# Kernel optimization log

Measured on AMD Instinct MI355X. Metric: run time of the kernel, lower is better.

The kernel has to match this reference:

```python
import jax, jax.numpy as jnp
import numpy as np

NUM_NODES = 50000
NUM_EDGES = 800000
NUM_LABEL_EDGES = 100000
F_IN, F_HID, F_OUT = 128, 128, 64


def gcn_conv(x, src, dst, W, b, n):
    # PyG GCNConv: h = x @ W; add self-loops; symmetric normalization
    # deg counted on destination (col), including self-loop (+1).
    h = x @ W
    deg = jax.ops.segment_sum(jnp.ones(src.shape, h.dtype), dst, num_segments=n) + 1.0
    dinv = jax.lax.rsqrt(deg)  # deg >= 1 always (self-loop)
    norm = dinv[src] * dinv[dst]                       # [E]
    agg = jax.ops.segment_sum(h[src] * norm[:, None], dst, num_segments=n)
    agg = agg + h * (dinv * dinv)[:, None]             # self-loop term dinv[i]^2 * h[i]
    return agg + b


def setup_inputs() -> dict:
    key = jax.random.key(0)
    ks = jax.random.split(key, 9)
    x = jax.random.normal(ks[0], (NUM_NODES, F_IN), dtype=jnp.float32)
    edge_index = jax.random.randint(ks[1], (2, NUM_EDGES), 0, NUM_NODES, dtype=jnp.int64)
    edge_label_index = jax.random.randint(ks[2], (2, NUM_LABEL_EDGES), 0, NUM_NODES, dtype=jnp.int64)
    def glorot(k, fi, fo):
        s = (6.0 / (fi + fo)) ** 0.5
        return jax.random.uniform(k, (fi, fo), jnp.float32, -s, s)
    return {
        "x": x,
        "edge_index": edge_index,
        "edge_label_index": edge_label_index,
        "W1": glorot(ks[3], F_IN, F_HID),  "b1": jnp.zeros((F_HID,), jnp.float32),
        "W2": glorot(ks[4], F_HID, F_HID), "b2": jnp.zeros((F_HID,), jnp.float32),
        "W3": glorot(ks[5], F_HID, F_OUT), "b3": jnp.zeros((F_OUT,), jnp.float32),
    }


def reference(x, edge_index, edge_label_index, W1, b1, W2, b2, W3, b3):
    src, dst = edge_index[0], edge_index[1]
    z = jax.nn.relu(gcn_conv(x, src, dst, W1, b1, NUM_NODES))
    z = jax.nn.relu(gcn_conv(z, src, dst, W2, b2, NUM_NODES))
    z = gcn_conv(z, src, dst, W3, b3, NUM_NODES)
    # decode: dot product of endpoint embeddings per label edge
    return jnp.sum(z[edge_label_index[0]] * z[edge_label_index[1]], axis=-1)
```

## Files before the change

kernel.cpp:

```cpp
#include <hip/hip_runtime.h>
#include <hip/hip_bf16.h>
#include <stdint.h>

#define NN 50000
#define NE 800000
#define NL 100000
#define SLOTS 64

#define NB 196
#define BSH 8
#define BCAP 5376

typedef __attribute__((ext_vector_type(8))) short bf16x8;
typedef __attribute__((ext_vector_type(4))) float f32x4;
typedef __attribute__((ext_vector_type(4))) unsigned int u32x4;
typedef __attribute__((ext_vector_type(2))) unsigned int u32x2;
typedef __attribute__((ext_vector_type(8))) unsigned short u16x8;

__device__ __forceinline__ float asf(unsigned int u) {
    union { unsigned int i; float f; } c; c.i = u; return c.f;
}
__device__ __forceinline__ float bflo(unsigned int x) { return asf(x << 16); }
__device__ __forceinline__ float bfhi(unsigned int x) { return asf(x & 0xffff0000u); }
__device__ __forceinline__ unsigned short f2bf(float f) {
    union { float f; unsigned int i; } c; c.f = f;
    unsigned int u = c.i + (0x7fffu + ((c.i >> 16) & 1u));
    return (unsigned short)(u >> 16);
}

__global__ void k_wprep(const float* __restrict__ W1, const float* __restrict__ W2,
                        const float* __restrict__ W3, unsigned short* __restrict__ Wt,
                        int* __restrict__ cursor) {
    int idx = blockIdx.x * 256 + threadIdx.x;
    if (idx < NB) cursor[idx] = 0;
    const float* W; unsigned short* O; int base, Mloc;
    if (idx < 16384)      { W = W1; O = Wt;         base = idx;         Mloc = 128; }
    else if (idx < 32768) { W = W2; O = Wt + 16384; base = idx - 16384; Mloc = 128; }
    else                  { W = W3; O = Wt + 32768; base = idx - 32768; Mloc = 64;  }
    int n = base >> 7, k = base & 127;
    O[base] = f2bf(W[k * Mloc + n]);
}

__global__ __launch_bounds__(256) void k_bin(
        const int* __restrict__ src, const int* __restrict__ dst,
        int* __restrict__ cursor, unsigned int* __restrict__ binbuf) {
    __shared__ int hcnt[NB];
    __shared__ int hbase[NB];
    __shared__ unsigned int epk[2048];
    int tid = threadIdx.x;
    if (tid < NB) hcnt[tid] = 0;
    __syncthreads();
    int e0 = blockIdx.x * 2048;
    int e1 = min(e0 + 2048, NE);
    for (int e = e0 + tid; e < e1; e += 256) {
        int d = dst[e], s = src[e];
        atomicAdd(&hcnt[d >> BSH], 1);
        epk[e - e0] = (unsigned int)s | ((unsigned int)d << 16);
    }
    __syncthreads();
    if (tid < NB) { hbase[tid] = atomicAdd(&cursor[tid], hcnt[tid]); hcnt[tid] = 0; }
    __syncthreads();
    for (int e = e0 + tid; e < e1; e += 256) {
        unsigned int pk = epk[e - e0];
        int b = (int)(pk >> 16) >> BSH;
        int p = hbase[b] + atomicAdd(&hcnt[b], 1);
        if (p < BCAP)
            __builtin_nontemporal_store(pk, &binbuf[(size_t)b * BCAP + p]);
    }
}

__global__ __launch_bounds__(256) void k_csr(
        const unsigned int* __restrict__ binbuf, const int* __restrict__ cursor,
        int* __restrict__ deg, unsigned short* __restrict__ colp) {
    __shared__ unsigned short lcol[256 * SLOTS];
    __shared__ int ldeg[256];
    int tid = threadIdx.x;
    int blk = blockIdx.x;
    int base = blk << BSH;
    int nNodes = min(256, NN - base);
    ldeg[tid] = 0;
    u32x4* lz = (u32x4*)lcol;
#pragma unroll
    for (int i = 0; i < 8; ++i) lz[i * 256 + tid] = (u32x4){0, 0, 0, 0};
    __syncthreads();
    int cnt = min(cursor[blk], BCAP);
    for (int e = tid; e < cnt; e += 256) {
        unsigned int pk = __builtin_nontemporal_load(&binbuf[(size_t)blk * BCAP + e]);
        int d = (int)(pk >> 16) - base;
        int p = atomicAdd(&ldeg[d], 1);
        if (p < SLOTS) {
            int pp = (p < 32) ? ((p & 3) * 8 + (p >> 2)) : p;
            lcol[d * SLOTS + pp] = (unsigned short)(pk & 0xffffu);
        }
    }
    __syncthreads();
    if (tid < nNodes) deg[base + tid] = ldeg[tid];
    u32x4* gout = (u32x4*)(colp + (size_t)base * SLOTS);
    const u32x4* lin = (const u32x4*)lcol;
    for (int i = tid; i < nNodes * 8; i += 256) gout[i] = lin[i];
}

__global__ __launch_bounds__(256) void k_gemm1(
        const float* __restrict__ A, const unsigned short* __restrict__ Wt,
        const int* __restrict__ deg, unsigned short* __restrict__ Outb, int N) {
    constexpr int K = 128;
    constexpr int NT = 8;
    int tid = threadIdx.x;
    int lane = tid & 63, wave = tid >> 6;
    int m = lane & 15, quad = lane >> 4;
    int rowA = blockIdx.x * 64 + wave * 16 + m;
    int rA = min(rowA, N - 1);

    bf16x8 afr[4];
    const float* p = A + (size_t)rA * K + quad * 8;
#pragma unroll
    for (int s = 0; s < 4; ++s) {
        float4 lo = *(const float4*)(p + s * 32);
        float4 hi = *(const float4*)(p + s * 32 + 4);
        bf16x8 r;
        r[0] = (short)f2bf(lo.x); r[1] = (short)f2bf(lo.y);
        r[2] = (short)f2bf(lo.z); r[3] = (short)f2bf(lo.w);
        r[4] = (short)f2bf(hi.x); r[5] = (short)f2bf(hi.y);
        r[6] = (short)f2bf(hi.z); r[7] = (short)f2bf(hi.w);
        afr[s] = r;
    }

    f32x4 acc[NT];
#pragma unroll
    for (int t = 0; t < NT; ++t) { acc[t][0] = 0.f; acc[t][1] = 0.f; acc[t][2] = 0.f; acc[t][3] = 0.f; }
#pragma unroll
    for (int t = 0; t < NT; ++t) {
        const unsigned short* wp = Wt + (size_t)(t * 16 + m) * K + quad * 8;
#pragma unroll
        for (int s = 0; s < 4; ++s) {
            bf16x8 bfr = *(const bf16x8*)(wp + s * 32);
            acc[t] = __builtin_amdgcn_mfma_f32_16x16x32_bf16(afr[s], bfr, acc[t], 0, 0, 0);
        }
    }

    int outRowBase = blockIdx.x * 64 + wave * 16 + quad * 4;
    float di[4];
#pragma unroll
    for (int i = 0; i < 4; ++i) di[i] = rsqrtf((float)deg[min(outRowBase + i, N - 1)] + 1.0f);
#pragma unroll
    for (int t = 0; t < NT; ++t)
#pragma unroll
        for (int i = 0; i < 4; ++i) {
            int rr = outRowBase + i;
            if (rr < N) Outb[(size_t)rr * 128 + t * 16 + m] = f2bf(acc[t][i] * di[i]);
        }
}

template <int M_>
__global__ __launch_bounds__(256, 8) void k_agg_gemm(
        const unsigned short* __restrict__ hs, const int* __restrict__ deg,
        const unsigned short* __restrict__ colp, const float* __restrict__ bias,
        const unsigned short* __restrict__ Wt, unsigned short* __restrict__ Outb) {
    constexpr int K = 128;
    constexpr int NT = M_ / 64;
    __shared__ __align__(16) unsigned short As[16][136];
    int tid = threadIdx.x;
    int lane = tid & 63, wave = tid >> 6;
    int tileBase = blockIdx.x * 16;
    int g = lane >> 4, c = lane & 15;
    const unsigned short* hc = hs + c * 8;
    int nodeB = tileBase + wave * 4;

    int degv[4], cnt[4];
#pragma unroll
    for (int t = 0; t < 4; ++t) { degv[t] = deg[nodeB + t]; cnt[t] = min(degv[t], SLOTS); }

    u16x8 sl = *(const u16x8*)(colp + (unsigned)nodeB * SLOTS + g * 8);
    unsigned int smk = (g == 0) ? 0xffffffffu : 0u;

#pragma unroll
    for (int t = 0; t < 4; ++t) {
        int r = wave * 4 + t;
        int node = nodeB + t;

        u32x4 sv = *(const u32x4*)(hc + (unsigned)node * K);
        u32x4 vv[4];
#pragma unroll
        for (int k2 = 0; k2 < 4; ++k2)
            vv[k2] = *(const u32x4*)(hc + (unsigned)sl[k2] * K);
        u16x8 sln = sl;
        if (t < 3) sln = *(const u16x8*)(colp + (unsigned)(node + 1) * SLOTS + g * 8);

        float acc[8];
#pragma unroll
        for (int k = 0; k < 4; ++k) {
            unsigned int xv = sv[k] & smk;
            acc[2 * k] = bflo(xv); acc[2 * k + 1] = bfhi(xv);
        }
#pragma unroll
        for (int k2 = 0; k2 < 4; ++k2) {
            unsigned int mk = (4 * k2 + g < cnt[t]) ? 0xffffffffu : 0u;
#pragma unroll
            for (int k = 0; k < 4; ++k) {
                unsigned int xv = vv[k2][k] & mk;
                acc[2 * k] += bflo(xv); acc[2 * k + 1] += bfhi(xv);
            }
        }
        if (cnt[t] > 16) {
#pragma unroll
            for (int k2 = 0; k2 < 4; ++k2)
                vv[k2] = *(const u32x4*)(hc + (unsigned)sl[k2 + 4] * K);
#pragma unroll
            for (int k2 = 0; k2 < 4; ++k2) {
                unsigned int mk = (16 + 4 * k2 + g < cnt[t]) ? 0xffffffffu : 0u;
#pragma unroll
                for (int k = 0; k < 4; ++k) {
                    unsigned int xv = vv[k2][k] & mk;
                    acc[2 * k] += bflo(xv); acc[2 * k + 1] += bfhi(xv);
                }
            }
        }
        if (cnt[t] > 32) {
            int mi = (lane < cnt[t]) ? (int)colp[(unsigned)node * SLOTS + lane] : 0;
            for (int j = 32; j < cnt[t]; j += 4) {
                int i0 = __shfl(mi, j + g, 64);
                u32x4 v0 = {0, 0, 0, 0};
                if (j + g < cnt[t]) v0 = *(const u32x4*)(hc + (unsigned)i0 * K);
#pragma unroll
                for (int k = 0; k < 4; ++k) {
                    acc[2 * k] += bflo(v0[k]); acc[2 * k + 1] += bfhi(v0[k]);
                }
            }
        }
        sl = sln;

#pragma unroll
        for (int k = 0; k < 8; ++k) {
            acc[k] += __shfl_xor(acc[k], 16, 64);
            acc[k] += __shfl_xor(acc[k], 32, 64);
        }
        if (g == 0) {
            float di = rsqrtf((float)degv[t] + 1.0f);
            const float4* bp = (const float4*)(bias + c * 8);
            float4 b0 = bp[0], b1 = bp[1];
            float bb[8] = {b0.x, b0.y, b0.z, b0.w, b1.x, b1.y, b1.z, b1.w};
            u32x4 pv;
#pragma unroll
            for (int k = 0; k < 4; ++k) {
                float o0 = fmaxf(di * acc[2 * k]     + bb[2 * k],     0.f);
                float o1 = fmaxf(di * acc[2 * k + 1] + bb[2 * k + 1], 0.f);
                pv[k] = (unsigned int)f2bf(o0) | ((unsigned int)f2bf(o1) << 16);
            }
            *(u32x4*)&As[r][c * 8] = pv;
        }
    }
    __syncthreads();

    int m = lane & 15, quad = lane >> 4;
    bf16x8 afr[4];
#pragma unroll
    for (int s = 0; s < 4; ++s)
        afr[s] = *(const bf16x8*)&As[m][s * 32 + quad * 8];

    f32x4 gacc[NT];
#pragma unroll
    for (int t = 0; t < NT; ++t) { gacc[t][0] = 0.f; gacc[t][1] = 0.f; gacc[t][2] = 0.f; gacc[t][3] = 0.f; }
#pragma unroll
    for (int t = 0; t < NT; ++t) {
        int ct = wave * NT + t;
        const unsigned short* wp = Wt + (size_t)(ct * 16 + m) * K + quad * 8;
#pragma unroll
        for (int s = 0; s < 4; ++s) {
            bf16x8 bfr = *(const bf16x8*)(wp + s * 32);
            gacc[t] = __builtin_amdgcn_mfma_f32_16x16x32_bf16(afr[s], bfr, gacc[t], 0, 0, 0);
        }
    }

    int rowBase = tileBase + quad * 4;
    float di[4];
#pragma unroll
    for (int i = 0; i < 4; ++i) di[i] = rsqrtf((float)deg[rowBase + i] + 1.0f);
#pragma unroll
    for (int t = 0; t < NT; ++t) {
        int ct = wave * NT + t;
#pragma unroll
        for (int i = 0; i < 4; ++i)
            Outb[(size_t)(rowBase + i) * M_ + ct * 16 + m] = f2bf(gacc[t][i] * di[i]);
    }
}

__global__ __launch_bounds__(256, 8) void k_agg64(
        const unsigned short* __restrict__ hs, const int* __restrict__ deg,
        const unsigned short* __restrict__ colp, const float* __restrict__ bias,
        unsigned short* __restrict__ out, int n) {
    int tid = threadIdx.x;
    int wave = tid >> 6, lane = tid & 63;
    int node = blockIdx.x * 4 + wave;
    int g = lane >> 4, c = lane & 15;
    const unsigned short* hc = hs + c * 4;

    int degv = deg[node];
    int cnt = min(degv, SLOTS);
    u16x8 sl = *(const u16x8*)(colp + (unsigned)node * SLOTS + g * 8);

    u32x2 sv = *(const u32x2*)(hc + (unsigned)node * 64);
    u32x2 vv[4];
#pragma unroll
    for (int k2 = 0; k2 < 4; ++k2)
        vv[k2] = *(const u32x2*)(hc + (unsigned)sl[k2] * 64);

    unsigned int smk = (g == 0) ? 0xffffffffu : 0u;
    float acc[4];
#pragma unroll
    for (int k = 0; k < 2; ++k) {
        unsigned int xv = sv[k] & smk;
        acc[2 * k] = bflo(xv); acc[2 * k + 1] = bfhi(xv);
    }
#pragma unroll
    for (int k2 = 0; k2 < 4; ++k2) {
        unsigned int mk = (4 * k2 + g < cnt) ? 0xffffffffu : 0u;
#pragma unroll
        for (int k = 0; k < 2; ++k) {
            unsigned int xv = vv[k2][k] & mk;
            acc[2 * k] += bflo(xv); acc[2 * k + 1] += bfhi(xv);
        }
    }
    if (cnt > 16) {
#pragma unroll
        for (int k2 = 0; k2 < 4; ++k2)
            vv[k2] = *(const u32x2*)(hc + (unsigned)sl[k2 + 4] * 64);
#pragma unroll
        for (int k2 = 0; k2 < 4; ++k2) {
            unsigned int mk = (16 + 4 * k2 + g < cnt) ? 0xffffffffu : 0u;
#pragma unroll
            for (int k = 0; k < 2; ++k) {
                unsigned int xv = vv[k2][k] & mk;
                acc[2 * k] += bflo(xv); acc[2 * k + 1] += bfhi(xv);
            }
        }
    }
    if (cnt > 32) {
        int mi = (lane < cnt) ? (int)colp[(unsigned)node * SLOTS + lane] : 0;
        for (int j = 32; j < cnt; j += 4) {
            int i0 = __shfl(mi, j + g, 64);
            u32x2 v0 = {0, 0};
            if (j + g < cnt) v0 = *(const u32x2*)(hc + (unsigned)i0 * 64);
#pragma unroll
            for (int k = 0; k < 2; ++k) {
                acc[2 * k] += bflo(v0[k]); acc[2 * k + 1] += bfhi(v0[k]);
            }
        }
    }
#pragma unroll
    for (int k = 0; k < 4; ++k) {
        acc[k] += __shfl_xor(acc[k], 16, 64);
        acc[k] += __shfl_xor(acc[k], 32, 64);
    }
    if (g == 0) {
        float di = rsqrtf((float)degv + 1.0f);
        float4 bb = *(const float4*)(bias + c * 4);
        u32x2 pv;
        pv[0] = (unsigned int)f2bf(di * acc[0] + bb.x) |
                ((unsigned int)f2bf(di * acc[1] + bb.y) << 16);
        pv[1] = (unsigned int)f2bf(di * acc[2] + bb.z) |
                ((unsigned int)f2bf(di * acc[3] + bb.w) << 16);
        *(u32x2*)(out + (size_t)node * 64 + c * 4) = pv;
    }
}

__global__ __launch_bounds__(256) void k_decode(
        const unsigned short* __restrict__ z, const int* __restrict__ ls,
        const int* __restrict__ ld, float* __restrict__ out, int nl) {
    int tid = threadIdx.x;
    int lane = tid & 63, wave = tid >> 6;
    int g = lane >> 3, c = lane & 7;
    int e = (blockIdx.x * 4 + wave) * 4 + (g >> 1);
    int row = (g & 1) ? ld[e] : ls[e];
    u32x4 v = *(const u32x4*)(z + (size_t)row * 64 + c * 8);
    u32x4 w;
#pragma unroll
    for (int k = 0; k < 4; ++k) w[k] = (unsigned int)__shfl_xor((int)v[k], 8, 64);
    float p = 0.f;
#pragma unroll
    for (int k = 0; k < 4; ++k)
        p += bflo(v[k]) * bflo(w[k]) + bfhi(v[k]) * bfhi(w[k]);
    p += __shfl_xor(p, 1, 64);
    p += __shfl_xor(p, 2, 64);
    p += __shfl_xor(p, 4, 64);
    if ((lane & 15) == 0) out[e] = p;
}


static inline size_t align256(size_t x) { return (x + 255) & ~(size_t)255; }

extern "C" void kernel_launch(void* const* d_in, const int* in_sizes, int n_in,
                              void* d_out, int out_size, void* d_ws, size_t ws_size,
                              hipStream_t stream) {
    const float* x  = (const float*)d_in[0];
    const int*   ei = (const int*)d_in[1];
    const int*   li = (const int*)d_in[2];
    const float* W1 = (const float*)d_in[3];
    const float* b1 = (const float*)d_in[4];
    const float* W2 = (const float*)d_in[5];
    const float* b2 = (const float*)d_in[6];
    const float* W3 = (const float*)d_in[7];
    const float* b3 = (const float*)d_in[8];
    float* out = (float*)d_out;

    const int* src = ei;
    const int* dst = ei + NE;
    const int* ls = li;
    const int* ld = li + NL;

    char* ws = (char*)d_ws;
    size_t off = 0;
    int* deg    = (int*)(ws + off); off += align256(NN * 4);
    int* cursor = (int*)(ws + off); off += align256(NB * 4);
    unsigned int* binbuf = (unsigned int*)(ws + off); off += align256((size_t)NB * BCAP * 4);
    unsigned short* colp = (unsigned short*)(ws + off); off += align256((size_t)NN * SLOTS * 2);
    unsigned short* Wtb  = (unsigned short*)(ws + off); off += align256(40960 * 2);
    unsigned short* bufA = (unsigned short*)(ws + off); off += align256((size_t)NN * 128 * 2);
    unsigned short* bufB = (unsigned short*)(ws + off); off += align256((size_t)NN * 128 * 2);
    unsigned short* bufZ = (unsigned short*)(ws + off); off += align256((size_t)NN * 64 * 2);

    k_wprep<<<160, 256, 0, stream>>>(W1, W2, W3, Wtb, cursor);
    k_bin<<<391, 256, 0, stream>>>(src, dst, cursor, binbuf);
    k_csr<<<NB, 256, 0, stream>>>(binbuf, cursor, deg, colp);

    k_gemm1<<<782, 256, 0, stream>>>(x, Wtb, deg, bufA, NN);
    k_agg_gemm<128><<<3125, 256, 0, stream>>>(bufA, deg, colp, b1, Wtb + 16384, bufB);
    k_agg_gemm<64><<<3125, 256, 0, stream>>>(bufB, deg, colp, b2, Wtb + 32768, bufA);
    k_agg64<<<12500, 256, 0, stream>>>(bufA, deg, colp, b3, bufZ, NN);
    k_decode<<<6250, 256, 0, stream>>>(bufZ, ls, ld, out, NL);
}
```

Measured before the change: 251.2 us.

## Fold self-loops into padded neighbor slots and gather branchlessly

The CSR build now fills empty neighbor slots with a sentinel index that points at a zeroed pad row, and writes each node's own index into the slot right after its last neighbor. The aggregation kernels can then gather a fixed first block of 24 slots with no masking and no separate self-term load, and the tail paths for high-degree nodes are unrolled. The layer-3 input buffer is offset inside bufA so that the 64-wide pad row lands on the already-zeroed row. The cost is always loading 24 slots, even for low-degree nodes, in exchange for removing per-element masks and branches.

```diff
diff --git a/kernel.cpp b/kernel.cpp
--- a/kernel.cpp
+++ b/kernel.cpp
@@ -6,6 +6,7 @@
 #define NE 800000
 #define NL 100000
 #define SLOTS 64
+#define PADROW 50000
 
 #define NB 196
 #define BSH 8
@@ -30,9 +31,12 @@
 
 __global__ void k_wprep(const float* __restrict__ W1, const float* __restrict__ W2,
                         const float* __restrict__ W3, unsigned short* __restrict__ Wt,
-                        int* __restrict__ cursor) {
+                        int* __restrict__ cursor, unsigned int* __restrict__ padA,
+                        unsigned int* __restrict__ padB) {
     int idx = blockIdx.x * 256 + threadIdx.x;
     if (idx < NB) cursor[idx] = 0;
+    if (idx < 64) padA[idx] = 0;
+    else if (idx < 128) padB[idx - 64] = 0;
     const float* W; unsigned short* O; int base, Mloc;
     if (idx < 16384)      { W = W1; O = Wt;         base = idx;         Mloc = 128; }
     else if (idx < 32768) { W = W2; O = Wt + 16384; base = idx - 16384; Mloc = 128; }
@@ -79,9 +83,11 @@
     int base = blk << BSH;
     int nNodes = min(256, NN - base);
     ldeg[tid] = 0;
+    const unsigned int fw = 0xC350C350u;
+    u32x4 fill = {fw, fw, fw, fw};
     u32x4* lz = (u32x4*)lcol;
 #pragma unroll
-    for (int i = 0; i < 8; ++i) lz[i * 256 + tid] = (u32x4){0, 0, 0, 0};
+    for (int i = 0; i < 8; ++i) lz[i * 256 + tid] = fill;
     __syncthreads();
     int cnt = min(cursor[blk], BCAP);
     for (int e = tid; e < cnt; e += 256) {
@@ -94,7 +100,15 @@
         }
     }
     __syncthreads();
-    if (tid < nNodes) deg[base + tid] = ldeg[tid];
+    if (tid < nNodes) {
+        int dv = ldeg[tid];
+        deg[base + tid] = dv;
+        if (dv < SLOTS) {
+            int pp = (dv < 32) ? ((dv & 3) * 8 + (dv >> 2)) : dv;
+            lcol[tid * SLOTS + pp] = (unsigned short)(base + tid);
+        }
+    }
+    __syncthreads();
     u32x4* gout = (u32x4*)(colp + (size_t)base * SLOTS);
     const u32x4* lin = (const u32x4*)lcol;
     for (int i = tid; i < nNodes * 8; i += 256) gout[i] = lin[i];
@@ -166,64 +180,54 @@
     const unsigned short* hc = hs + c * 8;
     int nodeB = tileBase + wave * 4;
 
-    int degv[4], cnt[4];
-#pragma unroll
-    for (int t = 0; t < 4; ++t) { degv[t] = deg[nodeB + t]; cnt[t] = min(degv[t], SLOTS); }
+    int4 dg = *(const int4*)(deg + nodeB);
+    int dgv[4] = {dg.x, dg.y, dg.z, dg.w};
 
     u16x8 sl = *(const u16x8*)(colp + (unsigned)nodeB * SLOTS + g * 8);
-    unsigned int smk = (g == 0) ? 0xffffffffu : 0u;
 
 #pragma unroll
     for (int t = 0; t < 4; ++t) {
-        int r = wave * 4 + t;
         int node = nodeB + t;
-
-        u32x4 sv = *(const u32x4*)(hc + (unsigned)node * K);
-        u32x4 vv[4];
-#pragma unroll
-        for (int k2 = 0; k2 < 4; ++k2)
+        int su = min(dgv[t] + 1, SLOTS);
+
+        u32x4 vv[6];
+#pragma unroll
+        for (int k2 = 0; k2 < 6; ++k2)
             vv[k2] = *(const u32x4*)(hc + (unsigned)sl[k2] * K);
         u16x8 sln = sl;
         if (t < 3) sln = *(const u16x8*)(colp + (unsigned)(node + 1) * SLOTS + g * 8);
 
         float acc[8];
 #pragma unroll
-        for (int k = 0; k < 4; ++k) {
-            unsigned int xv = sv[k] & smk;
-            acc[2 * k] = bflo(xv); acc[2 * k + 1] = bfhi(xv);
-        }
-#pragma unroll
-        for (int k2 = 0; k2 < 4; ++k2) {
-            unsigned int mk = (4 * k2 + g < cnt[t]) ? 0xffffffffu : 0u;
+        for (int k = 0; k < 8; ++k) acc[k] = 0.f;
+#pragma unroll
+        for (int k2 = 0; k2 < 6; ++k2)
 #pragma unroll
             for (int k = 0; k < 4; ++k) {
-                unsigned int xv = vv[k2][k] & mk;
-                acc[2 * k] += bflo(xv); acc[2 * k + 1] += bfhi(xv);
+                acc[2 * k]     += bflo(vv[k2][k]);
+                acc[2 * k + 1] += bfhi(vv[k2][k]);
             }
-        }
-        if (cnt[t] > 16) {
-#pragma unroll
-            for (int k2 = 0; k2 < 4; ++k2)
-                vv[k2] = *(const u32x4*)(hc + (unsigned)sl[k2 + 4] * K);
-#pragma unroll
-            for (int k2 = 0; k2 < 4; ++k2) {
-                unsigned int mk = (16 + 4 * k2 + g < cnt[t]) ? 0xffffffffu : 0u;
-#pragma unroll
-                for (int k = 0; k < 4; ++k) {
-                    unsigned int xv = vv[k2][k] & mk;
-                    acc[2 * k] += bflo(xv); acc[2 * k + 1] += bfhi(xv);
-                }
+        if (su > 24) {
+            u32x4 w0 = *(const u32x4*)(hc + (unsigned)sl[6] * K);
+            u32x4 w1 = *(const u32x4*)(hc + (unsigned)sl[7] * K);
+#pragma unroll
+            for (int k = 0; k < 4; ++k) {
+                acc[2 * k]     += bflo(w0[k]) + bflo(w1[k]);
+                acc[2 * k + 1] += bfhi(w0[k]) + bfhi(w1[k]);
             }
-        }
-        if (cnt[t] > 32) {
-            int mi = (lane < cnt[t]) ? (int)colp[(unsigned)node * SLOTS + lane] : 0;
-            for (int j = 32; j < cnt[t]; j += 4) {
-                int i0 = __shfl(mi, j + g, 64);
-                u32x4 v0 = {0, 0, 0, 0};
-                if (j + g < cnt[t]) v0 = *(const u32x4*)(hc + (unsigned)i0 * K);
-#pragma unroll
-                for (int k = 0; k < 4; ++k) {
-                    acc[2 * k] += bflo(v0[k]); acc[2 * k + 1] += bfhi(v0[k]);
+            if (su > 32) {
+                u16x8 s2 = *(const u16x8*)(colp + (unsigned)node * SLOTS + 32 + g * 8);
+#pragma unroll
+                for (int h = 0; h < 2; ++h) {
+                    u32x4 x0 = *(const u32x4*)(hc + (unsigned)s2[4 * h + 0] * K);
+                    u32x4 x1 = *(const u32x4*)(hc + (unsigned)s2[4 * h + 1] * K);
+                    u32x4 x2 = *(const u32x4*)(hc + (unsigned)s2[4 * h + 2] * K);
+                    u32x4 x3 = *(const u32x4*)(hc + (unsigned)s2[4 * h + 3] * K);
+#pragma unroll
+                    for (int k = 0; k < 4; ++k) {
+                        acc[2 * k]     += bflo(x0[k]) + bflo(x1[k]) + bflo(x2[k]) + bflo(x3[k]);
+                        acc[2 * k + 1] += bfhi(x0[k]) + bfhi(x1[k]) + bfhi(x2[k]) + bfhi(x3[k]);
+                    }
                 }
             }
         }
@@ -235,7 +239,7 @@
             acc[k] += __shfl_xor(acc[k], 32, 64);
         }
         if (g == 0) {
-            float di = rsqrtf((float)degv[t] + 1.0f);
+            float di = rsqrtf((float)dgv[t] + 1.0f);
             const float4* bp = (const float4*)(bias + c * 8);
             float4 b0 = bp[0], b1 = bp[1];
             float bb[8] = {b0.x, b0.y, b0.z, b0.w, b1.x, b1.y, b1.z, b1.w};
@@ -246,7 +250,7 @@
                 float o1 = fmaxf(di * acc[2 * k + 1] + bb[2 * k + 1], 0.f);
                 pv[k] = (unsigned int)f2bf(o0) | ((unsigned int)f2bf(o1) << 16);
             }
-            *(u32x4*)&As[r][c * 8] = pv;
+            *(u32x4*)&As[wave * 4 + t][c * 8] = pv;
         }
     }
     __syncthreads();
@@ -272,9 +276,11 @@
     }
 
     int rowBase = tileBase + quad * 4;
+    int4 dg2 = *(const int4*)(deg + rowBase);
+    int dgw[4] = {dg2.x, dg2.y, dg2.z, dg2.w};
     float di[4];
 #pragma unroll
-    for (int i = 0; i < 4; ++i) di[i] = rsqrtf((float)deg[rowBase + i] + 1.0f);
+    for (int i = 0; i < 4; ++i) di[i] = rsqrtf((float)dgw[i] + 1.0f);
 #pragma unroll
     for (int t = 0; t < NT; ++t) {
         int ct = wave * NT + t;
@@ -295,54 +301,43 @@
     const unsigned short* hc = hs + c * 4;
 
     int degv = deg[node];
-    int cnt = min(degv, SLOTS);
+    int su = min(degv + 1, SLOTS);
     u16x8 sl = *(const u16x8*)(colp + (unsigned)node * SLOTS + g * 8);
 
-    u32x2 sv = *(const u32x2*)(hc + (unsigned)node * 64);
-    u32x2 vv[4];
-#pragma unroll
-    for (int k2 = 0; k2 < 4; ++k2)
+    u32x2 vv[6];
+#pragma unroll
+    for (int k2 = 0; k2 < 6; ++k2)
         vv[k2] = *(const u32x2*)(hc + (unsigned)sl[k2] * 64);
 
-    unsigned int smk = (g == 0) ? 0xffffffffu : 0u;
-    float acc[4];
-#pragma unroll
-    for (int k = 0; k < 2; ++k) {
-        unsigned int xv = sv[k] & smk;
-        acc[2 * k] = bflo(xv); acc[2 * k + 1] = bfhi(xv);
-    }
-#pragma unroll
-    for (int k2 = 0; k2 < 4; ++k2) {
-        unsigned int mk = (4 * k2 + g < cnt) ? 0xffffffffu : 0u;
+    float acc[4] = {0.f, 0.f, 0.f, 0.f};
+#pragma unroll
+    for (int k2 = 0; k2 < 6; ++k2)
 #pragma unroll
         for (int k = 0; k < 2; ++k) {
-            unsigned int xv = vv[k2][k] & mk;
-            acc[2 * k] += bflo(xv); acc[2 * k + 1] += bfhi(xv);
-        }
-    }
-    if (cnt > 16) {
-#pragma unroll
-        for (int k2 = 0; k2 < 4; ++k2)
-            vv[k2] = *(const u32x2*)(hc + (unsigned)sl[k2 + 4] * 64);
-#pragma unroll
-        for (int k2 = 0; k2 < 4; ++k2) {
-            unsigned int mk = (16 + 4 * k2 + g < cnt) ? 0xffffffffu : 0u;
-#pragma unroll
-            for (int k = 0; k < 2; ++k) {
-                unsigned int xv = vv[k2][k] & mk;
-                acc[2 * k] += bflo(xv); acc[2 * k + 1] += bfhi(xv);
-            }
-        }
-    }
-    if (cnt > 32) {
-        int mi = (lane < cnt) ? (int)colp[(unsigned)node * SLOTS + lane] : 0;
-        for (int j = 32; j < cnt; j += 4) {
-            int i0 = __shfl(mi, j + g, 64);
-            u32x2 v0 = {0, 0};
-            if (j + g < cnt) v0 = *(const u32x2*)(hc + (unsigned)i0 * 64);
-#pragma unroll
-            for (int k = 0; k < 2; ++k) {
-                acc[2 * k] += bflo(v0[k]); acc[2 * k + 1] += bfhi(v0[k]);
+            acc[2 * k]     += bflo(vv[k2][k]);
+            acc[2 * k + 1] += bfhi(vv[k2][k]);
+        }
+    if (su > 24) {
+        u32x2 w0 = *(const u32x2*)(hc + (unsigned)sl[6] * 64);
+        u32x2 w1 = *(const u32x2*)(hc + (unsigned)sl[7] * 64);
+#pragma unroll
+        for (int k = 0; k < 2; ++k) {
+            acc[2 * k]     += bflo(w0[k]) + bflo(w1[k]);
+            acc[2 * k + 1] += bfhi(w0[k]) + bfhi(w1[k]);
+        }
+        if (su > 32) {
+            u16x8 s2 = *(const u16x8*)(colp + (unsigned)node * SLOTS + 32 + g * 8);
+#pragma unroll
+            for (int h = 0; h < 2; ++h) {
+                u32x2 x0 = *(const u32x2*)(hc + (unsigned)s2[4 * h + 0] * 64);
+                u32x2 x1 = *(const u32x2*)(hc + (unsigned)s2[4 * h + 1] * 64);
+                u32x2 x2 = *(const u32x2*)(hc + (unsigned)s2[4 * h + 2] * 64);
+                u32x2 x3 = *(const u32x2*)(hc + (unsigned)s2[4 * h + 3] * 64);
+#pragma unroll
+                for (int k = 0; k < 2; ++k) {
+                    acc[2 * k]     += bflo(x0[k]) + bflo(x1[k]) + bflo(x2[k]) + bflo(x3[k]);
+                    acc[2 * k + 1] += bfhi(x0[k]) + bfhi(x1[k]) + bfhi(x2[k]) + bfhi(x3[k]);
+                }
             }
         }
     }
@@ -414,17 +409,20 @@
     unsigned int* binbuf = (unsigned int*)(ws + off); off += align256((size_t)NB * BCAP * 4);
     unsigned short* colp = (unsigned short*)(ws + off); off += align256((size_t)NN * SLOTS * 2);
     unsigned short* Wtb  = (unsigned short*)(ws + off); off += align256(40960 * 2);
-    unsigned short* bufA = (unsigned short*)(ws + off); off += align256((size_t)NN * 128 * 2);
-    unsigned short* bufB = (unsigned short*)(ws + off); off += align256((size_t)NN * 128 * 2);
+    unsigned short* bufA = (unsigned short*)(ws + off); off += align256(((size_t)NN * 128 + 128) * 2);
+    unsigned short* bufB = (unsigned short*)(ws + off); off += align256(((size_t)NN * 128 + 128) * 2);
     unsigned short* bufZ = (unsigned short*)(ws + off); off += align256((size_t)NN * 64 * 2);
-
-    k_wprep<<<160, 256, 0, stream>>>(W1, W2, W3, Wtb, cursor);
+    unsigned short* h3 = bufA + (size_t)25000 * 128;
+
+    k_wprep<<<160, 256, 0, stream>>>(W1, W2, W3, Wtb, cursor,
+                                     (unsigned int*)(bufA + (size_t)PADROW * 128),
+                                     (unsigned int*)(bufB + (size_t)PADROW * 128));
     k_bin<<<391, 256, 0, stream>>>(src, dst, cursor, binbuf);
     k_csr<<<NB, 256, 0, stream>>>(binbuf, cursor, deg, colp);
 
     k_gemm1<<<782, 256, 0, stream>>>(x, Wtb, deg, bufA, NN);
     k_agg_gemm<128><<<3125, 256, 0, stream>>>(bufA, deg, colp, b1, Wtb + 16384, bufB);
-    k_agg_gemm<64><<<3125, 256, 0, stream>>>(bufB, deg, colp, b2, Wtb + 32768, bufA);
-    k_agg64<<<12500, 256, 0, stream>>>(bufA, deg, colp, b3, bufZ, NN);
+    k_agg_gemm<64><<<3125, 256, 0, stream>>>(bufB, deg, colp, b2, Wtb + 32768, h3);
+    k_agg64<<<12500, 256, 0, stream>>>(h3, deg, colp, b3, bufZ, NN);
     k_decode<<<6250, 256, 0, stream>>>(bufZ, ls, ld, out, NL);
 }
```

Result: faster. 232.0 us (-7.6%).
